# Optimization experiments

Hardware: AMD Instinct MI355X
Metric: run time of the kernel (lower is better)

## Reference

```python
import jax, jax.numpy as jnp
import numpy as np

B, LQ, LK, D, H, DK = 128, 32, 128, 1024, 16, 64


def setup_inputs() -> dict:
    key = jax.random.key(0)
    ks = jax.random.split(key, 10)
    Q_seq = jax.random.normal(ks[0], (B, LQ, D), dtype=jnp.float32)
    K_seq = jax.random.normal(ks[1], (B, LK, D), dtype=jnp.float32)
    V_seq = jax.random.normal(ks[2], (B, LK, D), dtype=jnp.float32)
    title_mask = (jax.random.uniform(ks[3], (B, LQ)) < 0.9).astype(jnp.float32)
    body_mask = (jax.random.uniform(ks[4], (B, LQ, LK)) < 0.9).astype(jnp.float32)
    s = 1.0 / np.sqrt(D)
    Wq = jax.random.uniform(ks[5], (H * DK, D), jnp.float32, -s, s)
    Wk = jax.random.uniform(ks[6], (H * DK, D), jnp.float32, -s, s)
    Wv = jax.random.uniform(ks[7], (H * DK, D), jnp.float32, -s, s)
    bq = jnp.zeros((H * DK,), jnp.float32)
    bk = jnp.zeros((H * DK,), jnp.float32)
    bv = jnp.zeros((H * DK,), jnp.float32)
    return {"Q_seq": Q_seq, "K_seq": K_seq, "V_seq": V_seq,
            "title_mask": title_mask, "body_mask": body_mask,
            "Wq": Wq, "bq": bq, "Wk": Wk, "bk": bk, "Wv": Wv, "bv": bv}


def reference(Q_seq, K_seq, V_seq, title_mask, body_mask, Wq, bq, Wk, bk, Wv, bv):
    b = Q_seq.shape[0]
    # concatenate title tokens onto keys/values: [B, LK+LQ, D]
    K_cat = jnp.concatenate([K_seq, Q_seq], axis=1)
    V_cat = jnp.concatenate([V_seq, Q_seq], axis=1)
    # mask: [B, LQ, LK+LQ]
    tmask_rep = jnp.broadcast_to(title_mask[:, None, :], (b, LQ, LQ))
    mask = jnp.concatenate([body_mask, tmask_rep], axis=2) * title_mask[:, :, None]
    # projections -> [B, H, len, DK]
    Qh = (Q_seq @ Wq.T + bq).reshape(b, LQ, H, DK).transpose(0, 2, 1, 3)
    Kh = (K_cat @ Wk.T + bk).reshape(b, LK + LQ, H, DK).transpose(0, 2, 1, 3)
    Vh = (V_cat @ Wv.T + bv).reshape(b, LK + LQ, H, DK).transpose(0, 2, 1, 3)
    # custom exp-based masked attention (non-softmax normalization)
    scores = jnp.einsum('bhqd,bhkd->bhqk', Qh, Kh) / np.sqrt(float(DK))
    scores = jnp.exp(scores) * mask[:, None, :, :]
    attn = scores / (jnp.sum(scores, axis=-1, keepdims=True) + 1e-8)
    ctx = jnp.einsum('bhqk,bhkd->bhqd', attn, Vh)
    return ctx.transpose(0, 2, 1, 3).reshape(b, LQ, H * DK)
```

## Files before the change

### kernel.cpp

```cpp
#include <hip/hip_runtime.h>

typedef _Float16 f16;
typedef _Float16 f16x2 __attribute__((ext_vector_type(2)));
typedef _Float16 f16x4 __attribute__((ext_vector_type(4)));
typedef _Float16 f16x8 __attribute__((ext_vector_type(8)));
typedef float f32x4v __attribute__((ext_vector_type(4)));

#define AS1 __attribute__((address_space(1)))
#define AS3 __attribute__((address_space(3)))

__device__ __forceinline__ void gload_lds16(const f16* g, f16* l) {
  __builtin_amdgcn_global_load_lds((const AS1 unsigned int*)g,
                                   (AS3 unsigned int*)l, 16, 0, 0);
}

__global__ __launch_bounds__(256) void prep_kernel(
    const float* __restrict__ Q_seq, const float* __restrict__ K_seq,
    const float* __restrict__ V_seq,
    const float* __restrict__ Wq, const float* __restrict__ Wk,
    const float* __restrict__ Wv,
    f16* __restrict__ Qb, f16* __restrict__ Kb, f16* __restrict__ Vb,
    f16* __restrict__ Wqb, f16* __restrict__ Wkb, f16* __restrict__ Wvb)
{
  const long long g = (long long)blockIdx.x * 256 + threadIdx.x;
  const float* s;
  f16* d;
  if (g < 524288) {
    s = Q_seq + g * 8; d = Qb + g * 8;
  } else if (g < 2621440) {
    long long e = (g - 524288) * 8; s = K_seq + e; d = Kb + e;
  } else if (g < 4718592) {
    long long e = (g - 2621440) * 8; s = V_seq + e; d = Vb + e;
  } else if (g < 4849664) {
    long long e = (g - 4718592) * 8; s = Wq + e; d = Wqb + e;
  } else if (g < 4980736) {
    long long e = (g - 4849664) * 8; s = Wk + e; d = Wkb + e;
  } else {
    long long e = (g - 4980736) * 8; s = Wv + e; d = Wvb + e;
  }
  float4 v0 = *(const float4*)s;
  float4 v1 = *(const float4*)(s + 4);
  f16x8 o;
  o[0] = (f16)v0.x; o[1] = (f16)v0.y; o[2] = (f16)v0.z; o[3] = (f16)v0.w;
  o[4] = (f16)v1.x; o[5] = (f16)v1.y; o[6] = (f16)v1.z; o[7] = (f16)v1.w;
  *(f16x8*)d = o;
}

__device__ __forceinline__ void gemm_tile_256(
    const f16* __restrict__ A, const f16* __restrict__ W,
    const float* __restrict__ bias, f16* __restrict__ C,
    int m0, int n0, int rowShift, int outStride, int rowOff,
    f16* sbuf)
{
  const int t = threadIdx.x;
  const int w = t >> 6, lane = t & 63;
  const int wr = w >> 2, wc = w & 3;
  const int fr = lane & 15, g = lane >> 4;
  const int lrow = lane >> 3;
  const int kgr = (lane & 7) ^ lrow;

  const f16* aSrc[4];
  const f16* bSrc[4];
#pragma unroll
  for (int s = 0; s < 4; ++s) {
    aSrc[s] = A + (long long)(m0 + (w * 4 + s) * 8 + lrow) * 1024 + kgr * 8;
    bSrc[s] = W + (long long)(n0 + (w * 4 + s) * 8 + lrow) * 1024 + kgr * 8;
  }

#define STAGE(tile)                                                          \
  {                                                                          \
    f16* ab_ = sbuf + (((tile) & 1) << 15);                                  \
    const int ko_ = (tile) * 64;                                             \
    _Pragma("unroll") for (int s = 0; s < 4; ++s)                            \
        gload_lds16(aSrc[s] + ko_, ab_ + (w * 4 + s) * 512);                 \
    _Pragma("unroll") for (int s = 0; s < 4; ++s)                            \
        gload_lds16(bSrc[s] + ko_, ab_ + 16384 + (w * 4 + s) * 512);         \
  }

  const int gk0 = ((0 + g) ^ (fr & 7)) * 8;
  const int gk1 = ((4 + g) ^ (fr & 7)) * 8;
  const int aoff = (wr * 128 + fr) * 64;
  const int boff = (wc * 64 + fr) * 64;

  f32x4v acc[8][4];
#pragma unroll
  for (int i = 0; i < 8; ++i)
#pragma unroll
    for (int j = 0; j < 4; ++j) acc[i][j] = (f32x4v){0.f, 0.f, 0.f, 0.f};

  STAGE(0);
  STAGE(1);

  for (int tt = 0; tt < 16; ++tt) {
    if (tt < 15) {
      asm volatile("s_waitcnt vmcnt(8)" ::: "memory");
    } else {
      asm volatile("s_waitcnt vmcnt(0)" ::: "memory");
    }
    __builtin_amdgcn_s_barrier();
    __builtin_amdgcn_sched_barrier(0);

    const f16* ab = sbuf + ((tt & 1) << 15);
    const f16* bb = ab + 16384;

    f16x8 av0[8], bv0[4];
#pragma unroll
    for (int i = 0; i < 8; ++i)
      av0[i] = *(const f16x8*)(ab + aoff + i * 1024 + gk0);
#pragma unroll
    for (int j = 0; j < 4; ++j)
      bv0[j] = *(const f16x8*)(bb + boff + j * 1024 + gk0);
    asm volatile("s_waitcnt lgkmcnt(0)" ::: "memory");
    __builtin_amdgcn_sched_barrier(0);
    __builtin_amdgcn_s_setprio(1);
#pragma unroll
    for (int i = 0; i < 8; ++i)
#pragma unroll
      for (int j = 0; j < 4; ++j)
        acc[i][j] = __builtin_amdgcn_mfma_f32_16x16x32_f16(av0[i], bv0[j],
                                                           acc[i][j], 0, 0, 0);
    __builtin_amdgcn_s_setprio(0);

    f16x8 av1[8], bv1[4];
#pragma unroll
    for (int i = 0; i < 8; ++i)
      av1[i] = *(const f16x8*)(ab + aoff + i * 1024 + gk1);
#pragma unroll
    for (int j = 0; j < 4; ++j)
      bv1[j] = *(const f16x8*)(bb + boff + j * 1024 + gk1);
    asm volatile("s_waitcnt lgkmcnt(0)" ::: "memory");
    __builtin_amdgcn_sched_barrier(0);
    __builtin_amdgcn_s_barrier();
    __builtin_amdgcn_sched_barrier(0);
    if (tt < 14) STAGE(tt + 2);
    __builtin_amdgcn_sched_barrier(0);
    __builtin_amdgcn_s_setprio(1);
#pragma unroll
    for (int i = 0; i < 8; ++i)
#pragma unroll
      for (int j = 0; j < 4; ++j)
        acc[i][j] = __builtin_amdgcn_mfma_f32_16x16x32_f16(av1[i], bv1[j],
                                                           acc[i][j], 0, 0, 0);
    __builtin_amdgcn_s_setprio(0);
  }
#undef STAGE

  f16* Cs = sbuf;
  float bn[4];
#pragma unroll
  for (int j = 0; j < 4; ++j) bn[j] = bias[n0 + wc * 64 + j * 16 + fr];
#pragma unroll
  for (int i = 0; i < 8; ++i) {
#pragma unroll
    for (int j = 0; j < 4; ++j) {
#pragma unroll
      for (int v = 0; v < 4; ++v) {
        int row = wr * 128 + i * 16 + g * 4 + v;
        int col = wc * 64 + j * 16 + fr;
        Cs[row * 256 + (col ^ (((row >> 2) & 7) << 3))] =
            (f16)(acc[i][j][v] + bn[j]);
      }
    }
  }
  __syncthreads();

  const int rowMask = (1 << rowShift) - 1;
  const int row = t >> 1, half = t & 1;
  const int csw = ((row >> 2) & 7) << 3;
  const int arow = m0 + row;
  const int orow = (arow >> rowShift) * outStride + (arow & rowMask) + rowOff;
  f16* dst = C + (long long)orow * 1024 + n0 + half * 128;
  const f16* srcr = Cs + row * 256;
#pragma unroll
  for (int c = 0; c < 16; ++c)
    *(f16x8*)(dst + c * 8) = *(const f16x8*)(srcr + ((half * 128 + c * 8) ^ csw));
}

__global__ __launch_bounds__(512, 1) void gemm_kv2(
    const f16* __restrict__ Kb, const f16* __restrict__ Wkb,
    const float* __restrict__ bk, f16* __restrict__ Kh,
    const f16* __restrict__ Vb, const f16* __restrict__ Wvb,
    const float* __restrict__ bv, f16* __restrict__ Vh)
{
  __shared__ __align__(16) f16 sbuf[65536];
  const int bid = blockIdx.x;
  const int v = (bid & 7) * 64 + (bid >> 3);
  const int z = v >> 8, rem = v & 255;
  const int by = rem >> 2, bx = rem & 3;
  const f16* A = z ? Vb : Kb;
  const f16* W = z ? Wvb : Wkb;
  const float* bias = z ? bv : bk;
  f16* C = z ? Vh : Kh;
  gemm_tile_256(A, W, bias, C, by * 256, bx * 256, 7, 160, 0, sbuf);
}

__global__ __launch_bounds__(512, 1) void gemm_q3(
    const f16* __restrict__ Qb,
    const f16* __restrict__ Wqb, const f16* __restrict__ Wkb,
    const f16* __restrict__ Wvb,
    const float* __restrict__ bq, const float* __restrict__ bk,
    const float* __restrict__ bv,
    f16* __restrict__ Qh, f16* __restrict__ Kh, f16* __restrict__ Vh)
{
  __shared__ __align__(16) f16 sbuf[65536];
  const int bid = blockIdx.x;
  const int v = (bid & 7) * 24 + (bid >> 3);
  const int z = v >> 6, rem = v & 63;
  const int by = rem >> 2, bx = rem & 3;
  const f16* W = (z == 0) ? Wqb : (z == 1) ? Wkb : Wvb;
  const float* bias = (z == 0) ? bq : (z == 1) ? bk : bv;
  f16* C = (z == 0) ? Qh : (z == 1) ? Kh : Vh;
  const int outStride = (z == 0) ? 32 : 160;
  const int rowOff = (z == 0) ? 0 : 128;
  gemm_tile_256(Qb, W, bias, C, by * 256, bx * 256, 5, outStride, rowOff, sbuf);
}

__global__ __launch_bounds__(256) void attn_kernel(
    const f16* __restrict__ Qh, const f16* __restrict__ Kh,
    const f16* __restrict__ Vh,
    const float* __restrict__ title, const float* __restrict__ body,
    float* __restrict__ out)
{
  __shared__ __align__(16) f16 Qs[32 * 72];
  __shared__ __align__(16) f16 Ks[160 * 72];
  __shared__ __align__(16) f16 Vs[160 * 68];
  __shared__ float rs[4][32];
  __shared__ float invs[32];

  const int bh = blockIdx.x, b = bh >> 4, h = bh & 15;
  const int t = threadIdx.x, w = t >> 6, lane = t & 63;
  const int c = lane & 15, g = lane >> 4;

  const long long qbase = ((long long)(b * 32) << 10) + h * 64;
  const long long kbase = ((long long)(b * 160) << 10) + h * 64;

  {
    int row = t >> 3, ch = t & 7;
    *(f16x8*)(Qs + row * 72 + ch * 8) =
        *(const f16x8*)(Qh + qbase + (long long)row * 1024 + ch * 8);
  }
#pragma unroll
  for (int r = 0; r < 5; ++r) {
    int i = t + r * 256;
    int row = i >> 3, ch = i & 7;
    *(f16x8*)(Ks + row * 72 + ch * 8) =
        *(const f16x8*)(Kh + kbase + (long long)row * 1024 + ch * 8);
    f16x8 vv = *(const f16x8*)(Vh + kbase + (long long)row * 1024 + ch * 8);
    f16x4 vlo = __builtin_shufflevector(vv, vv, 0, 1, 2, 3);
    f16x4 vhi = __builtin_shufflevector(vv, vv, 4, 5, 6, 7);
    *(f16x4*)(Vs + row * 68 + ch * 8) = vlo;
    *(f16x4*)(Vs + row * 68 + ch * 8 + 4) = vhi;
  }
  __syncthreads();

  f16x8 qf[2][2];
#pragma unroll
  for (int qt = 0; qt < 2; ++qt)
#pragma unroll
    for (int s = 0; s < 2; ++s)
      qf[qt][s] = *(const f16x8*)(Qs + (qt * 16 + c) * 72 + s * 32 + g * 8);

  const int cnt = (w < 2) ? 3 : 2;
  const int tile0 = (w < 2) ? w * 3 : 6 + (w - 2) * 2;

  f16x4 pp[3][2];
  float rsum[2] = {0.f, 0.f};

#pragma unroll
  for (int i = 0; i < 3; ++i) {
    if (i < cnt) {
      const int kt = tile0 + i;
      f16x8 kf0 = *(const f16x8*)(Ks + (kt * 16 + c) * 72 + 0 + g * 8);
      f16x8 kf1 = *(const f16x8*)(Ks + (kt * 16 + c) * 72 + 32 + g * 8);
#pragma unroll
      for (int qt = 0; qt < 2; ++qt) {
        f32x4v s4 = (f32x4v){0.f, 0.f, 0.f, 0.f};
        s4 = __builtin_amdgcn_mfma_f32_16x16x32_f16(kf0, qf[qt][0], s4, 0, 0, 0);
        s4 = __builtin_amdgcn_mfma_f32_16x16x32_f16(kf1, qf[qt][1], s4, 0, 0, 0);
        float4 m4;
        if (kt < 8) {
          m4 = *(const float4*)(body +
                ((long long)(b * 32 + qt * 16 + c)) * 128 + kt * 16 + 4 * g);
        } else {
          m4 = *(const float4*)(title + b * 32 + (kt - 8) * 16 + 4 * g);
        }
        float e0 = __expf(s4[0] * 0.125f) * m4.x;
        float e1 = __expf(s4[1] * 0.125f) * m4.y;
        float e2 = __expf(s4[2] * 0.125f) * m4.z;
        float e3 = __expf(s4[3] * 0.125f) * m4.w;
        rsum[qt] += (e0 + e1) + (e2 + e3);
        f16x4 p4;
        p4.x = (f16)e0; p4.y = (f16)e1; p4.z = (f16)e2; p4.w = (f16)e3;
        pp[i][qt] = p4;
      }
    }
  }

#pragma unroll
  for (int qt = 0; qt < 2; ++qt) {
    rsum[qt] += __shfl_xor(rsum[qt], 16);
    rsum[qt] += __shfl_xor(rsum[qt], 32);
  }
  if (lane < 16) {
    rs[w][c] = rsum[0];
    rs[w][16 + c] = rsum[1];
  }
  __syncthreads();

  f16* Ps = Ks;
#pragma unroll
  for (int i = 0; i < 3; ++i) {
    if (i < cnt) {
      const int kt = tile0 + i;
#pragma unroll
      for (int qt = 0; qt < 2; ++qt)
        *(f16x4*)(Ps + (qt * 16 + c) * 168 + kt * 16 + 4 * g) = pp[i][qt];
    }
  }
  if (t < 32) {
    float ssum = rs[0][t] + rs[1][t] + rs[2][t] + rs[3][t];
    invs[t] = title[b * 32 + t] / (ssum + 1e-8f);
  }
  __syncthreads();

  f32x4v o[2] = {(f32x4v){0.f, 0.f, 0.f, 0.f}, (f32x4v){0.f, 0.f, 0.f, 0.f}};
#pragma unroll
  for (int s = 0; s < 5; ++s) {
    f16x8 vf;
#pragma unroll
    for (int j = 0; j < 8; ++j)
      vf[j] = Vs[(32 * s + 8 * g + j) * 68 + 16 * w + c];
#pragma unroll
    for (int qt = 0; qt < 2; ++qt) {
      f16x8 pf = *(const f16x8*)(Ps + (qt * 16 + c) * 168 + s * 32 + g * 8);
      o[qt] = __builtin_amdgcn_mfma_f32_16x16x32_f16(pf, vf, o[qt], 0, 0, 0);
    }
  }

#pragma unroll
  for (int qt = 0; qt < 2; ++qt) {
#pragma unroll
    for (int v = 0; v < 4; ++v) {
      int q = qt * 16 + 4 * g + v;
      out[((long long)(b * 32 + q) << 10) + h * 64 + 16 * w + c] =
          o[qt][v] * invs[q];
    }
  }
}

extern "C" void kernel_launch(void* const* d_in, const int* in_sizes, int n_in,
                              void* d_out, int out_size, void* d_ws, size_t ws_size,
                              hipStream_t stream) {
  const float* Q_seq = (const float*)d_in[0];
  const float* K_seq = (const float*)d_in[1];
  const float* V_seq = (const float*)d_in[2];
  const float* title = (const float*)d_in[3];
  const float* body  = (const float*)d_in[4];
  const float* Wq = (const float*)d_in[5];
  const float* bq = (const float*)d_in[6];
  const float* Wk = (const float*)d_in[7];
  const float* bk = (const float*)d_in[8];
  const float* Wv = (const float*)d_in[9];
  const float* bv = (const float*)d_in[10];
  float* out = (float*)d_out;

  f16* ws = (f16*)d_ws;
  f16* Qb  = ws;
  f16* Kb  = Qb + 4194304;
  f16* Vb  = Kb + 16777216;
  f16* Wqb = Vb + 16777216;
  f16* Wkb = Wqb + 1048576;
  f16* Wvb = Wkb + 1048576;
  f16* Qh  = Wvb + 1048576;
  f16* Kh  = Qh + 4194304;
  f16* Vh  = Kh + 20971520;

  prep_kernel<<<19968, 256, 0, stream>>>(Q_seq, K_seq, V_seq, Wq, Wk, Wv,
                                         Qb, Kb, Vb, Wqb, Wkb, Wvb);
  gemm_kv2<<<512, 512, 0, stream>>>(Kb, Wkb, bk, Kh, Vb, Wvb, bv, Vh);
  gemm_q3<<<192, 512, 0, stream>>>(Qb, Wqb, Wkb, Wvb, bq, bk, bv,
                                   Qh, Kh, Vh);
  attn_kernel<<<2048, 256, 0, stream>>>(Qh, Kh, Vh, title, body, out);
}
```

Measured before the change: 188.1 us.

## Merge KV and Q projection GEMMs into one launch and prefetch second k-half LDS reads

The separate K/V and Q projection GEMM launches become a single 704-block kernel with an XCD-aware block remap. This removes a launch and the tail gap between the two grids. Inside the GEMM tile, the LDS reads for the second k-half are now issued before the first MFMA batch, with a partial lgkmcnt wait, so LDS latency overlaps with matrix math. That raises register pressure, since both operand sets are live at once, which could cause spills at 512 threads.

Result: faster. 183.7 us (-2.4%).

```diff
diff --git a/kernel.cpp b/kernel.cpp
--- a/kernel.cpp
+++ b/kernel.cpp
@@ -103,14 +103,22 @@
     const f16* ab = sbuf + ((tt & 1) << 15);
     const f16* bb = ab + 16384;
 
-    f16x8 av0[8], bv0[4];
+    f16x8 av0[8], bv0[4], av1[8], bv1[4];
 #pragma unroll
     for (int i = 0; i < 8; ++i)
       av0[i] = *(const f16x8*)(ab + aoff + i * 1024 + gk0);
 #pragma unroll
     for (int j = 0; j < 4; ++j)
       bv0[j] = *(const f16x8*)(bb + boff + j * 1024 + gk0);
-    asm volatile("s_waitcnt lgkmcnt(0)" ::: "memory");
+    __builtin_amdgcn_sched_barrier(0);
+#pragma unroll
+    for (int i = 0; i < 8; ++i)
+      av1[i] = *(const f16x8*)(ab + aoff + i * 1024 + gk1);
+#pragma unroll
+    for (int j = 0; j < 4; ++j)
+      bv1[j] = *(const f16x8*)(bb + boff + j * 1024 + gk1);
+
+    asm volatile("s_waitcnt lgkmcnt(12)" ::: "memory");
     __builtin_amdgcn_sched_barrier(0);
     __builtin_amdgcn_s_setprio(1);
 #pragma unroll
@@ -121,13 +129,6 @@
                                                            acc[i][j], 0, 0, 0);
     __builtin_amdgcn_s_setprio(0);
 
-    f16x8 av1[8], bv1[4];
-#pragma unroll
-    for (int i = 0; i < 8; ++i)
-      av1[i] = *(const f16x8*)(ab + aoff + i * 1024 + gk1);
-#pragma unroll
-    for (int j = 0; j < 4; ++j)
-      bv1[j] = *(const f16x8*)(bb + boff + j * 1024 + gk1);
     asm volatile("s_waitcnt lgkmcnt(0)" ::: "memory");
     __builtin_amdgcn_sched_barrier(0);
     __builtin_amdgcn_s_barrier();
@@ -176,26 +177,9 @@
     *(f16x8*)(dst + c * 8) = *(const f16x8*)(srcr + ((half * 128 + c * 8) ^ csw));
 }
 
-__global__ __launch_bounds__(512, 1) void gemm_kv2(
-    const f16* __restrict__ Kb, const f16* __restrict__ Wkb,
-    const float* __restrict__ bk, f16* __restrict__ Kh,
-    const f16* __restrict__ Vb, const f16* __restrict__ Wvb,
-    const float* __restrict__ bv, f16* __restrict__ Vh)
-{
-  __shared__ __align__(16) f16 sbuf[65536];
-  const int bid = blockIdx.x;
-  const int v = (bid & 7) * 64 + (bid >> 3);
-  const int z = v >> 8, rem = v & 255;
-  const int by = rem >> 2, bx = rem & 3;
-  const f16* A = z ? Vb : Kb;
-  const f16* W = z ? Wvb : Wkb;
-  const float* bias = z ? bv : bk;
-  f16* C = z ? Vh : Kh;
-  gemm_tile_256(A, W, bias, C, by * 256, bx * 256, 7, 160, 0, sbuf);
-}
-
-__global__ __launch_bounds__(512, 1) void gemm_q3(
-    const f16* __restrict__ Qb,
+__global__ __launch_bounds__(512, 1) void gemm_all(
+    const f16* __restrict__ Qb, const f16* __restrict__ Kb,
+    const f16* __restrict__ Vb,
     const f16* __restrict__ Wqb, const f16* __restrict__ Wkb,
     const f16* __restrict__ Wvb,
     const float* __restrict__ bq, const float* __restrict__ bk,
@@ -204,15 +188,35 @@
 {
   __shared__ __align__(16) f16 sbuf[65536];
   const int bid = blockIdx.x;
-  const int v = (bid & 7) * 24 + (bid >> 3);
-  const int z = v >> 6, rem = v & 63;
-  const int by = rem >> 2, bx = rem & 3;
-  const f16* W = (z == 0) ? Wqb : (z == 1) ? Wkb : Wvb;
-  const float* bias = (z == 0) ? bq : (z == 1) ? bk : bv;
-  f16* C = (z == 0) ? Qh : (z == 1) ? Kh : Vh;
-  const int outStride = (z == 0) ? 32 : 160;
-  const int rowOff = (z == 0) ? 0 : 128;
-  gemm_tile_256(Qb, W, bias, C, by * 256, bx * 256, 5, outStride, rowOff, sbuf);
+  const int v = (bid & 7) * 88 + (bid >> 3);
+
+  const f16* A;
+  const f16* W;
+  const float* bias;
+  f16* C;
+  int m0, n0, rowShift, outStride, rowOff;
+
+  if (v < 512) {
+    const int z = v >> 8, rem = v & 255;
+    A = z ? Vb : Kb;
+    W = z ? Wvb : Wkb;
+    bias = z ? bv : bk;
+    C = z ? Vh : Kh;
+    m0 = (rem >> 2) * 256; n0 = (rem & 3) * 256;
+    rowShift = 7; outStride = 160; rowOff = 0;
+  } else {
+    const int u = v - 512;
+    const int z = u >> 6, rem = u & 63;
+    A = Qb;
+    W = (z == 0) ? Wqb : (z == 1) ? Wkb : Wvb;
+    bias = (z == 0) ? bq : (z == 1) ? bk : bv;
+    C = (z == 0) ? Qh : (z == 1) ? Kh : Vh;
+    m0 = (rem >> 2) * 256; n0 = (rem & 3) * 256;
+    rowShift = 5;
+    outStride = (z == 0) ? 32 : 160;
+    rowOff = (z == 0) ? 0 : 128;
+  }
+  gemm_tile_256(A, W, bias, C, m0, n0, rowShift, outStride, rowOff, sbuf);
 }
 
 __global__ __launch_bounds__(256) void attn_kernel(
@@ -377,8 +381,7 @@
 
   prep_kernel<<<19968, 256, 0, stream>>>(Q_seq, K_seq, V_seq, Wq, Wk, Wv,
                                          Qb, Kb, Vb, Wqb, Wkb, Wvb);
-  gemm_kv2<<<512, 512, 0, stream>>>(Kb, Wkb, bk, Kh, Vb, Wvb, bv, Vh);
-  gemm_q3<<<192, 512, 0, stream>>>(Qb, Wqb, Wkb, Wvb, bq, bk, bv,
-                                   Qh, Kh, Vh);
+  gemm_all<<<704, 512, 0, stream>>>(Qb, Kb, Vb, Wqb, Wkb, Wvb,
+                                    bq, bk, bv, Qh, Kh, Vh);
   attn_kernel<<<2048, 256, 0, stream>>>(Qh, Kh, Vh, title, body, out);
 }
```
